# Optimization experiments

Hardware: AMD Instinct MI355X
Metric: run time of the kernel (lower is better)

## Reference

```python
import jax, jax.numpy as jnp
import numpy as np

B, N, K = 16, 2048, 20
EPS = 1e-5
SLOPE = 0.2  # LeakyReLU negative slope


def _lrelu(x):
    return jnp.where(x >= 0, x, SLOPE * x)


def _bn(x, g, b, axes):
    # BatchNorm in training mode (batch statistics), channel-last layout
    m = x.mean(axes, keepdims=True)
    v = x.var(axes, keepdims=True)
    return (x - m) * jax.lax.rsqrt(v + EPS) * g + b


def _graph_features(pts, k):
    # pts: [B, N, C] -> edge features [B, N, k, 2C] = concat(x_j - x_i, x_i)
    xx = jnp.sum(pts * pts, axis=-1)                       # [B, N]
    inner = jnp.einsum('bnc,bmc->bnm', pts, pts)           # [B, N, N]
    neg_d = 2.0 * inner - xx[:, :, None] - xx[:, None, :]  # -||x_i - x_j||^2
    _, idx = jax.lax.top_k(neg_d, k)                       # [B, N, k]
    xj = jax.vmap(lambda p, i: p[i])(pts, idx)             # [B, N, k, C]
    xi = pts[:, :, None, :]                                # [B, N, 1, C]
    return jnp.concatenate([xj - xi, jnp.broadcast_to(xi, xj.shape)], axis=-1)


def _forward(x, conv_w, conv_g, conv_b, w1, b1, g1, bt1, w2, b2, g2, bt2,
             w3, b3, g3, bt3, w4, b4, w5, b5):
    feat = _graph_features(x, K)                           # [B, N, K, 6]
    # 1x1 Conv2d (bias=False) + BN2d + LeakyReLU, then max over neighbors
    h = jnp.einsum('bnkc,oc->bnko', feat, conv_w)          # [B, N, K, 64]
    h = _lrelu(_bn(h, conv_g, conv_b, (0, 1, 2)))
    h = h.max(axis=2)                                      # [B, N, 64]
    # DBR blocks: Linear + BN1d + LeakyReLU over points
    h = _lrelu(_bn(h @ w1 + b1, g1, bt1, (0, 1)))          # [B, N, 64]
    h = _lrelu(_bn(h @ w2 + b2, g2, bt2, (0, 1)))          # [B, N, 128]
    h = _lrelu(_bn(h @ w3 + b3, g3, bt3, (0, 1)))          # [B, N, 128]
    h = h.max(axis=1)                                      # MaxChannel -> [B, 128]
    h = _lrelu(h @ w4 + b4)                                # DbR -> [B, 512]
    return h @ w5 + b5                                     # [B, 2*Z_DIM=256]


def setup_inputs() -> dict:
    key = jax.random.key(0)
    ks = jax.random.split(key, 8)
    rn = lambda k, s, sc: (jax.random.normal(k, s, jnp.float32) * sc)
    return {
        'x': jax.random.normal(ks[0], (B, N, 3), jnp.float32),
        'conv_w': rn(ks[1], (64, 6), 0.3),
        'conv_g': jnp.ones(64, jnp.float32), 'conv_b': jnp.zeros(64, jnp.float32),
        'w1': rn(ks[2], (64, 64), 0.1), 'b1': jnp.zeros(64, jnp.float32),
        'g1': jnp.ones(64, jnp.float32), 'bt1': jnp.zeros(64, jnp.float32),
        'w2': rn(ks[3], (64, 128), 0.1), 'b2': jnp.zeros(128, jnp.float32),
        'g2': jnp.ones(128, jnp.float32), 'bt2': jnp.zeros(128, jnp.float32),
        'w3': rn(ks[4], (128, 128), 0.1), 'b3': jnp.zeros(128, jnp.float32),
        'g3': jnp.ones(128, jnp.float32), 'bt3': jnp.zeros(128, jnp.float32),
        'w4': rn(ks[5], (128, 512), 0.05), 'b4': jnp.zeros(512, jnp.float32),
        'w5': rn(ks[6], (512, 256), 0.05), 'b5': jnp.zeros(256, jnp.float32),
    }


def reference(x, conv_w, conv_g, conv_b, w1, b1, g1, bt1, w2, b2, g2, bt2,
              w3, b3, g3, bt3, w4, b4, w5, b5):
    return _forward(x, conv_w, conv_g, conv_b, w1, b1, g1, bt1, w2, b2, g2, bt2,
                    w3, b3, g3, bt3, w4, b4, w5, b5)
```

## Files before the change

kernel.cpp:

```cpp
#include <hip/hip_runtime.h>
#include <math.h>

#define NB   16
#define NPTS 2048
#define KNBR 20
#define NCH  16
#define CHSZ (NPTS/NCH)
#define NROWS (NB*NPTS)
#define CONV_M ((double)(NB)*(double)(NPTS)*(double)(KNBR))
#define ROW_M  ((double)NROWS)
#define BN_EPS 1e-5
#define LSLOPE 0.2f

__device__ __forceinline__ float lrelu(float v) { return v >= 0.f ? v : LSLOPE * v; }

__device__ __forceinline__ float4 stage4(float px, float py, float pz)
{
    return make_float4(px + px, py + py, pz + pz,
                       -fmaf(px, px, fmaf(py, py, pz * pz)));
}

__device__ __forceinline__ float dist_eval(float4 q, float4 c)
{
    float t = fmaf(c.x, q.x, fmaf(c.y, q.y, fmaf(c.z, q.z, q.w)));
    return t + c.w;
}

__device__ __forceinline__ void pair_insert_sorted(float (&bestv)[KNBR], float t0, float t1)
{
#pragma unroll
    for (int j = 0; j < KNBR; ++j) {
        float bj = bestv[j];
        float nb  = fmaxf(bj, t0);
        float nt0 = __builtin_amdgcn_fmed3f(bj, t0, t1);
        float nt1 = fminf(bj, t1);
        bestv[j] = nb;
        t0 = nt0; t1 = nt1;
    }
}

__global__ __launch_bounds__(256) void knn_part(const float* __restrict__ x,
                                                float* __restrict__ P)
{
    __shared__ float4 cpt[2*CHSZ];
    __shared__ float4 qpt[256];
    const int b  = blockIdx.x >> 6;
    const int qg = (blockIdx.x >> 3) & 7;
    const int c0 = blockIdx.x & 7;
    const float* xb = x + (size_t)b * NPTS * 3;
    {
        const int half = threadIdx.x >> 7;
        const int jloc = threadIdx.x & (CHSZ - 1);
        const int j = (c0 + half*8) * CHSZ + jloc;
        cpt[threadIdx.x] = stage4(xb[j*3+0], xb[j*3+1], xb[j*3+2]);
        const int n = qg * 256 + threadIdx.x;
        float px = xb[n*3+0], py = xb[n*3+1], pz = xb[n*3+2];
        qpt[threadIdx.x] = make_float4(px, py, pz,
                                       -fmaf(px, px, fmaf(py, py, pz * pz)));
    }
    __syncthreads();
    const float4 q = qpt[threadIdx.x];
    float bA[KNBR], bB[KNBR];
#pragma unroll
    for (int j = 0; j < KNBR; ++j) { bA[j] = -__builtin_inff(); bB[j] = -__builtin_inff(); }
    for (int m = 0; m < CHSZ; m += 2) {
        float dA0 = dist_eval(q, cpt[m]);
        float dA1 = dist_eval(q, cpt[m+1]);
        float dB0 = dist_eval(q, cpt[CHSZ + m]);
        float dB1 = dist_eval(q, cpt[CHSZ + m+1]);
        float tA0 = fmaxf(dA0, dA1), tA1 = fminf(dA0, dA1);
        float tB0 = fmaxf(dB0, dB1), tB1 = fminf(dB0, dB1);
#pragma unroll
        for (int j = 0; j < KNBR; ++j) {
            float aj = bA[j], bj = bB[j];
            float nbA = fmaxf(aj, tA0);
            float nbB = fmaxf(bj, tB0);
            float nA0 = __builtin_amdgcn_fmed3f(aj, tA0, tA1);
            float nB0 = __builtin_amdgcn_fmed3f(bj, tB0, tB1);
            float nA1 = fminf(aj, tA1);
            float nB1 = fminf(bj, tB1);
            bA[j] = nbA; bB[j] = nbB;
            tA0 = nA0; tA1 = nA1; tB0 = nB0; tB1 = nB1;
        }
    }
    const size_t bq = (size_t)b * NPTS + qg * 256 + threadIdx.x;
#pragma unroll
    for (int i = 0; i < KNBR; ++i) {
        P[(size_t)(c0 * KNBR + i) * NROWS + bq]       = bA[i];
        P[(size_t)((c0+8) * KNBR + i) * NROWS + bq]   = bB[i];
    }
}

__global__ __launch_bounds__(256) void knn_merge(const float* __restrict__ P,
                                                 float* __restrict__ thresh)
{
    const size_t bq = (size_t)blockIdx.x * 256 + threadIdx.x;
    float bestv[KNBR];
#pragma unroll
    for (int j = 0; j < KNBR; ++j) bestv[j] = -__builtin_inff();
    for (int c = 0; c < NCH; ++c) {
        for (int i = 0; i < KNBR; i += 2) {
            float d0 = P[(size_t)(c * KNBR + i)     * NROWS + bq];
            float d1 = P[(size_t)(c * KNBR + i + 1) * NROWS + bq];
            if (!__any(d0 > bestv[KNBR-1])) break;
            pair_insert_sorted(bestv, d0, d1);
        }
    }
    thresh[bq] = bestv[KNBR-1];
}

__global__ __launch_bounds__(256) void idxfeat_kernel(const float* __restrict__ x,
        const float* __restrict__ thresh, const float* __restrict__ conv_w,
        float* __restrict__ maxh, float* __restrict__ minh, double* __restrict__ S)
{
    __shared__ float4 pts[NPTS];
    __shared__ unsigned short idxl[32][KNBR];
    __shared__ float  featw[4][KNBR][6];
    __shared__ double sred[4][27];
    const int b  = blockIdx.x >> 6;
    const int qg = blockIdx.x & 63;
    const int wv = threadIdx.x >> 6, lane = threadIdx.x & 63;
    const float* xb = x + (size_t)b * NPTS * 3;
    for (int i = threadIdx.x; i < NPTS; i += 256)
        pts[i] = stage4(xb[i*3+0], xb[i*3+1], xb[i*3+2]);
    __syncthreads();
    const unsigned long long below = (1ull << lane) - 1ull;
    for (int qi = 0; qi < 8; ++qi) {
        const int p = wv * 8 + qi;
        const int n = qg * 32 + p;
        const float4 qc = pts[n];
        const float4 q = make_float4(0.5f*qc.x, 0.5f*qc.y, 0.5f*qc.z, qc.w);
        const float th = thresh[(size_t)b * NPTS + n];
        int cnt = 0;
        for (int it = 0; it < NPTS/64; ++it) {
            float d = dist_eval(q, pts[it*64 + lane]);
            const bool hit = (d >= th);
            unsigned long long mask = __ballot(hit);
            int pos = cnt + __popcll(mask & below);
            if (hit && pos < KNBR)
                idxl[p][pos] = (unsigned short)(it*64 + lane);
            cnt += __popcll(mask);
        }
    }
    __syncthreads();
    float cw[6];
#pragma unroll
    for (int c = 0; c < 6; ++c) cw[c] = conv_w[lane*6 + c];
    int pa_ = 0, pb_ = 0;
    if (lane >= 6 && lane < 27) {
        int t = lane - 6, a = 0;
        while (t >= 6 - a) { t -= 6 - a; ++a; }
        pa_ = a; pb_ = a + t;
    }
    double acc = 0.0;
    for (int i = 0; i < 8; ++i) {
        const int p = wv * 8 + i;
        const int nn = qg * 32 + p;
        const size_t bp = (size_t)b * NPTS + nn;
        const float4 Ci = pts[nn];
        const float xi0 = 0.5f*Ci.x, xi1 = 0.5f*Ci.y, xi2 = 0.5f*Ci.z;
        float f0=0,f1=0,f2=0,f3=0,f4=0,f5=0;
        if (lane < KNBR) {
            const float4 Cj = pts[idxl[p][lane]];
            f0 = 0.5f*(Cj.x - Ci.x);
            f1 = 0.5f*(Cj.y - Ci.y);
            f2 = 0.5f*(Cj.z - Ci.z);
            f3 = xi0; f4 = xi1; f5 = xi2;
        }
        __syncthreads();
        if (lane < KNBR) {
            featw[wv][lane][0]=f0; featw[wv][lane][1]=f1; featw[wv][lane][2]=f2;
            featw[wv][lane][3]=f3; featw[wv][lane][4]=f4; featw[wv][lane][5]=f5;
        }
        __syncthreads();
        float vmax = -__builtin_inff(), vmin = __builtin_inff();
#pragma unroll
        for (int k = 0; k < KNBR; ++k) {
            float h = featw[wv][k][0] * cw[0];
            h = fmaf(featw[wv][k][1], cw[1], h);
            h = fmaf(featw[wv][k][2], cw[2], h);
            h = fmaf(featw[wv][k][3], cw[3], h);
            h = fmaf(featw[wv][k][4], cw[4], h);
            h = fmaf(featw[wv][k][5], cw[5], h);
            vmax = fmaxf(vmax, h); vmin = fminf(vmin, h);
        }
        maxh[bp*64 + lane] = vmax;
        minh[bp*64 + lane] = vmin;
        if (lane < 6) {
            double s = 0;
#pragma unroll
            for (int k = 0; k < KNBR; ++k) s += (double)featw[wv][k][lane];
            acc += s;
        } else if (lane < 27) {
            double s = 0;
#pragma unroll
            for (int k = 0; k < KNBR; ++k)
                s += (double)featw[wv][k][pa_] * (double)featw[wv][k][pb_];
            acc += s;
        }
    }
    if (lane < 27) sred[wv][lane] = acc;
    __syncthreads();
    if (threadIdx.x < 27) {
        double tot = sred[0][threadIdx.x] + sred[1][threadIdx.x]
                   + sred[2][threadIdx.x] + sred[3][threadIdx.x];
        atomicAdd(&S[threadIdx.x], tot);
    }
}

__global__ void stats0_kernel(const double* __restrict__ S, const float* __restrict__ conv_w,
        const float* __restrict__ g, const float* __restrict__ bb,
        float* __restrict__ scale, float* __restrict__ shift)
{
    const int o = threadIdx.x;
    double w[6];
#pragma unroll
    for (int c = 0; c < 6; ++c) w[c] = (double)conv_w[o*6 + c];
    double mean = 0.0;
#pragma unroll
    for (int c = 0; c < 6; ++c) mean += w[c] * S[c];
    mean /= CONV_M;
    double ey2 = 0.0;
    int t = 6;
#pragma unroll
    for (int a = 0; a < 6; ++a)
#pragma unroll
        for (int b2 = a; b2 < 6; ++b2) {
            double coef = (a == b2) ? 1.0 : 2.0;
            ey2 += coef * w[a] * w[b2] * S[t];
            ++t;
        }
    ey2 /= CONV_M;
    double var = ey2 - mean * mean;
    double sc = (double)g[o] / sqrt(var + BN_EPS);
    scale[o] = (float)sc;
    shift[o] = (float)((double)bb[o] - mean * sc);
}

__global__ void statsL_kernel(const double* __restrict__ sum, const double* __restrict__ sq,
        const float* __restrict__ g, const float* __restrict__ bt,
        float* __restrict__ scale, float* __restrict__ shift, int C)
{
    const int o = threadIdx.x;
    if (o >= C) return;
    double m = sum[o] / ROW_M;
    double v = sq[o] / ROW_M - m * m;
    double sc = (double)g[o] / sqrt(v + BN_EPS);
    scale[o] = (float)sc;
    shift[o] = (float)((double)bt[o] - m * sc);
}

template<int K, int N, bool SEL, bool POOLOUT>
__global__ __launch_bounds__(256) void mlp_gemm(const float* __restrict__ A,
        const float* __restrict__ A2, const float* __restrict__ sc_,
        const float* __restrict__ sh_, const float* __restrict__ W,
        const float* __restrict__ bias, float* __restrict__ Y,
        double* __restrict__ sum, double* __restrict__ sq,
        float* __restrict__ pmax_g, float* __restrict__ pmin_g)
{
    constexpr int CPT = N / 16;
    __shared__ float As[64 * 64];
    __shared__ float Ws[64 * N];
    const int tid = threadIdx.x;
    const int row0 = blockIdx.x * 64;
    const int ct = tid & 15, rt = tid >> 4;
    float acc[4][CPT];
#pragma unroll
    for (int rr = 0; rr < 4; ++rr)
#pragma unroll
        for (int cc = 0; cc < CPT; ++cc) acc[rr][cc] = bias[ct*CPT + cc];

    for (int kk = 0; kk < K/64; ++kk) {
        if (kk) __syncthreads();
#pragma unroll
        for (int i = 0; i < 4; ++i) {
            const int f   = i * 256 + tid;
            const int k4  = f & 15;
            const int row = f >> 4;
            const int kg  = kk*64 + k4*4;
            float4 m = *(const float4*)(A + (size_t)(row0+row)*K + kg);
            const float4 s4 = *(const float4*)(sc_ + kg);
            const float4 h4 = *(const float4*)(sh_ + kg);
            if (SEL) {
                float4 m2 = *(const float4*)(A2 + (size_t)(row0+row)*K + kg);
                m.x = s4.x >= 0.f ? m.x : m2.x;
                m.y = s4.y >= 0.f ? m.y : m2.y;
                m.z = s4.z >= 0.f ? m.z : m2.z;
                m.w = s4.w >= 0.f ? m.w : m2.w;
            }
            const int rsw = row ^ ((k4 & 7) << 2);
            As[(k4*4+0)*64 + rsw] = lrelu(fmaf(s4.x, m.x, h4.x));
            As[(k4*4+1)*64 + rsw] = lrelu(fmaf(s4.y, m.y, h4.y));
            As[(k4*4+2)*64 + rsw] = lrelu(fmaf(s4.z, m.z, h4.z));
            As[(k4*4+3)*64 + rsw] = lrelu(fmaf(s4.w, m.w, h4.w));
        }
#pragma unroll
        for (int i = 0; i < N/16; ++i) {
            const int f    = i * 256 + tid;
            const int col4 = f & (N/4 - 1);
            const int krow = f / (N/4);
            *(float4*)(&Ws[krow*N + col4*4]) =
                *(const float4*)(W + (size_t)(kk*64 + krow)*N + col4*4);
        }
        __syncthreads();
#pragma unroll 4
        for (int k = 0; k < 64; ++k) {
            const int sw = ((k >> 2) & 7) << 2;
            const float4 a0 = *(const float4*)(&As[k*64 + ((rt*4) ^ sw)]);
            float a_[4] = {a0.x, a0.y, a0.z, a0.w};
            float w_[CPT];
#pragma unroll
            for (int v = 0; v < CPT/4; ++v) {
                const float4 wv4 = *(const float4*)(&Ws[k*N + ct*CPT + v*4]);
                w_[v*4+0] = wv4.x; w_[v*4+1] = wv4.y; w_[v*4+2] = wv4.z; w_[v*4+3] = wv4.w;
            }
#pragma unroll
            for (int rr = 0; rr < 4; ++rr)
#pragma unroll
                for (int cc = 0; cc < CPT; ++cc)
                    acc[rr][cc] = fmaf(a_[rr], w_[cc], acc[rr][cc]);
        }
    }
    if (!POOLOUT) {
#pragma unroll
        for (int rr = 0; rr < 4; ++rr) {
            float* yo = Y + (size_t)(row0 + rt*4 + rr)*N + ct*CPT;
#pragma unroll
            for (int v = 0; v < CPT/4; ++v)
                *(float4*)(yo + v*4) = make_float4(acc[rr][v*4+0], acc[rr][v*4+1],
                                                   acc[rr][v*4+2], acc[rr][v*4+3]);
        }
    }
    __syncthreads();
    float* cr  = As;
    float* pmx = As + 512;
    float* pmn = Ws;
    if (tid < 2*N) cr[tid] = 0.f;
    if (POOLOUT) {
#pragma unroll
        for (int cc = 0; cc < CPT; ++cc) {
            float vmax = fmaxf(fmaxf(acc[0][cc], acc[1][cc]), fmaxf(acc[2][cc], acc[3][cc]));
            float vmin = fminf(fminf(acc[0][cc], acc[1][cc]), fminf(acc[2][cc], acc[3][cc]));
            pmx[rt*N + ct*CPT + cc] = vmax;
            pmn[rt*N + ct*CPT + cc] = vmin;
        }
    }
    __syncthreads();
#pragma unroll
    for (int cc = 0; cc < CPT; ++cc) {
        float s = acc[0][cc] + acc[1][cc] + acc[2][cc] + acc[3][cc];
        float q = fmaf(acc[0][cc], acc[0][cc], 0.f);
        q = fmaf(acc[1][cc], acc[1][cc], q);
        q = fmaf(acc[2][cc], acc[2][cc], q);
        q = fmaf(acc[3][cc], acc[3][cc], q);
        atomicAdd(&cr[ct*CPT + cc], s);
        atomicAdd(&cr[N + ct*CPT + cc], q);
    }
    float rm = 0.f, rn = 0.f;
    if (POOLOUT && tid < N) {
        rm = pmx[tid]; rn = pmn[tid];
#pragma unroll
        for (int r = 1; r < 16; ++r) {
            rm = fmaxf(rm, pmx[r*N + tid]);
            rn = fminf(rn, pmn[r*N + tid]);
        }
    }
    __syncthreads();
    if (tid < N) {
        atomicAdd(&sum[tid], (double)cr[tid]);
        atomicAdd(&sq[tid],  (double)cr[N + tid]);
        if (POOLOUT) {
            pmax_g[(size_t)blockIdx.x * N + tid] = rm;
            pmin_g[(size_t)blockIdx.x * N + tid] = rn;
        }
    }
}

__global__ __launch_bounds__(256) void headpool_kernel(const float* __restrict__ pmax_g,
        const float* __restrict__ pmin_g, const float* __restrict__ s3,
        const float* __restrict__ t3, const float* __restrict__ w4,
        const float* __restrict__ b4, const float* __restrict__ w5,
        const float* __restrict__ b5, float* __restrict__ out)
{
    __shared__ float xr[128];
    __shared__ float hh[512];
    const int b = blockIdx.x, t = threadIdx.x;
    if (t < 128) {
        const float* pm = pmax_g + (size_t)b * 32 * 128 + t;
        const float* pn = pmin_g + (size_t)b * 32 * 128 + t;
        float m = pm[0], n_ = pn[0];
#pragma unroll
        for (int r = 1; r < 32; ++r) {
            m  = fmaxf(m,  pm[r*128]);
            n_ = fminf(n_, pn[r*128]);
        }
        const float sc = s3[t], sh = t3[t];
        xr[t] = lrelu(sc >= 0.f ? fmaf(sc, m, sh) : fmaf(sc, n_, sh));
    }
    __syncthreads();
    float h0 = b4[t], h1 = b4[t + 256];
    for (int c = 0; c < 128; ++c) {
        float xc = xr[c];
        h0 = fmaf(xc, w4[c*512 + t],       h0);
        h1 = fmaf(xc, w4[c*512 + t + 256], h1);
    }
    hh[t]       = lrelu(h0);
    hh[t + 256] = lrelu(h1);
    __syncthreads();
    float acc = b5[t];
    for (int c = 0; c < 512; ++c)
        acc = fmaf(hh[c], w5[c*256 + t], acc);
    out[b*256 + t] = acc;
}

extern "C" void kernel_launch(void* const* d_in, const int* in_sizes, int n_in,
                              void* d_out, int out_size, void* d_ws, size_t ws_size,
                              hipStream_t stream)
{
    const float* x      = (const float*)d_in[0];
    const float* conv_w = (const float*)d_in[1];
    const float* conv_g = (const float*)d_in[2];
    const float* conv_b = (const float*)d_in[3];
    const float* w1  = (const float*)d_in[4];
    const float* b1  = (const float*)d_in[5];
    const float* g1  = (const float*)d_in[6];
    const float* bt1 = (const float*)d_in[7];
    const float* w2  = (const float*)d_in[8];
    const float* b2  = (const float*)d_in[9];
    const float* g2  = (const float*)d_in[10];
    const float* bt2 = (const float*)d_in[11];
    const float* w3  = (const float*)d_in[12];
    const float* b3  = (const float*)d_in[13];
    const float* g3  = (const float*)d_in[14];
    const float* bt3 = (const float*)d_in[15];
    const float* w4  = (const float*)d_in[16];
    const float* b4  = (const float*)d_in[17];
    const float* w5  = (const float*)d_in[18];
    const float* b5  = (const float*)d_in[19];

    char* p = (char*)d_ws;
    auto take = [&](size_t bytes) -> char* {
        char* r = p; p += (bytes + 255) & ~(size_t)255; return r;
    };
    double* S    = (double*)take(27 * 8);
    double* sum1 = (double*)take(64 * 8);
    double* sq1  = (double*)take(64 * 8);
    double* sum2 = (double*)take(128 * 8);
    double* sq2  = (double*)take(128 * 8);
    double* sum3 = (double*)take(128 * 8);
    double* sq3  = (double*)take(128 * 8);
    size_t zero_bytes = (size_t)(p - (char*)d_ws);
    float* scale0 = (float*)take(64 * 4);
    float* shift0 = (float*)take(64 * 4);
    float* scale1 = (float*)take(64 * 4);
    float* shift1 = (float*)take(64 * 4);
    float* scale2 = (float*)take(128 * 4);
    float* shift2 = (float*)take(128 * 4);
    float* scale3 = (float*)take(128 * 4);
    float* shift3 = (float*)take(128 * 4);
    float* pmaxg  = (float*)take((size_t)512 * 128 * 4);
    float* pming  = (float*)take((size_t)512 * 128 * 4);
    float* thresh = (float*)take((size_t)NROWS * 4);
    float* mm     = (float*)take((size_t)NROWS * 128 * 4);
    float* maxh   = mm;
    float* minh   = mm + (size_t)NROWS * 64;
    float* y1     = (float*)take((size_t)NROWS * 64 * 4);
    float* y2     = (float*)take((size_t)NROWS * 128 * 4);
    float* P      = mm;

    hipMemsetAsync(d_ws, 0, zero_bytes, stream);
    knn_part  <<<dim3(NB * 8 * 8),   dim3(256), 0, stream>>>(x, P);
    knn_merge <<<dim3(NROWS / 256),  dim3(256), 0, stream>>>(P, thresh);
    idxfeat_kernel<<<dim3(NB * 64),  dim3(256), 0, stream>>>(x, thresh, conv_w, maxh, minh, S);
    stats0_kernel<<<dim3(1),         dim3(64),  0, stream>>>(S, conv_w, conv_g, conv_b, scale0, shift0);

    mlp_gemm<64,64,true,false>   <<<dim3(512), dim3(256), 0, stream>>>(maxh, minh, scale0, shift0, w1, b1, y1, sum1, sq1, nullptr, nullptr);
    statsL_kernel                <<<dim3(1),   dim3(64),  0, stream>>>(sum1, sq1, g1, bt1, scale1, shift1, 64);
    mlp_gemm<64,128,false,false> <<<dim3(512), dim3(256), 0, stream>>>(y1, y1, scale1, shift1, w2, b2, y2, sum2, sq2, nullptr, nullptr);
    statsL_kernel                <<<dim3(1),   dim3(128), 0, stream>>>(sum2, sq2, g2, bt2, scale2, shift2, 128);
    mlp_gemm<128,128,false,true> <<<dim3(512), dim3(256), 0, stream>>>(y2, y2, scale2, shift2, w3, b3, nullptr, sum3, sq3, pmaxg, pming);
    statsL_kernel                <<<dim3(1),   dim3(128), 0, stream>>>(sum3, sq3, g3, bt3, scale3, shift3, 128);

    headpool_kernel<<<dim3(NB),      dim3(256), 0, stream>>>(pmaxg, pming, scale3, shift3, w4, b4, w5, b5, (float*)d_out);
}
```

Before: 409.1 us.

## Replace partial-sort kNN with per-wave radix bisection and fold BN stats into consumers

Drops the two-pass kNN (per-chunk top-20 insertion sort plus merge kernel). Each wavefront now keeps its query's 2048 distances in registers as order-preserving unsigned keys and bisects on the key value with ballot/popcount to find the 20th-largest threshold, then gathers indices as before. The separate BN statistics kernels are also removed: each GEMM block and the head kernel recompute scale/shift from the accumulated sums, which cuts launches and a global round trip. In exchange, every block redoes the small double-precision stats math, and the bisection can take up to 32 passes of 32 ballots per query while holding 32 key registers per lane.

```diff
diff --git a/kernel.cpp b/kernel.cpp
--- a/kernel.cpp
+++ b/kernel.cpp
@@ -4,8 +4,6 @@
 #define NB   16
 #define NPTS 2048
 #define KNBR 20
-#define NCH  16
-#define CHSZ (NPTS/NCH)
 #define NROWS (NB*NPTS)
 #define CONV_M ((double)(NB)*(double)(NPTS)*(double)(KNBR))
 #define ROW_M  ((double)NROWS)
@@ -26,91 +24,8 @@
     return t + c.w;
 }
 
-__device__ __forceinline__ void pair_insert_sorted(float (&bestv)[KNBR], float t0, float t1)
-{
-#pragma unroll
-    for (int j = 0; j < KNBR; ++j) {
-        float bj = bestv[j];
-        float nb  = fmaxf(bj, t0);
-        float nt0 = __builtin_amdgcn_fmed3f(bj, t0, t1);
-        float nt1 = fminf(bj, t1);
-        bestv[j] = nb;
-        t0 = nt0; t1 = nt1;
-    }
-}
-
-__global__ __launch_bounds__(256) void knn_part(const float* __restrict__ x,
-                                                float* __restrict__ P)
-{
-    __shared__ float4 cpt[2*CHSZ];
-    __shared__ float4 qpt[256];
-    const int b  = blockIdx.x >> 6;
-    const int qg = (blockIdx.x >> 3) & 7;
-    const int c0 = blockIdx.x & 7;
-    const float* xb = x + (size_t)b * NPTS * 3;
-    {
-        const int half = threadIdx.x >> 7;
-        const int jloc = threadIdx.x & (CHSZ - 1);
-        const int j = (c0 + half*8) * CHSZ + jloc;
-        cpt[threadIdx.x] = stage4(xb[j*3+0], xb[j*3+1], xb[j*3+2]);
-        const int n = qg * 256 + threadIdx.x;
-        float px = xb[n*3+0], py = xb[n*3+1], pz = xb[n*3+2];
-        qpt[threadIdx.x] = make_float4(px, py, pz,
-                                       -fmaf(px, px, fmaf(py, py, pz * pz)));
-    }
-    __syncthreads();
-    const float4 q = qpt[threadIdx.x];
-    float bA[KNBR], bB[KNBR];
-#pragma unroll
-    for (int j = 0; j < KNBR; ++j) { bA[j] = -__builtin_inff(); bB[j] = -__builtin_inff(); }
-    for (int m = 0; m < CHSZ; m += 2) {
-        float dA0 = dist_eval(q, cpt[m]);
-        float dA1 = dist_eval(q, cpt[m+1]);
-        float dB0 = dist_eval(q, cpt[CHSZ + m]);
-        float dB1 = dist_eval(q, cpt[CHSZ + m+1]);
-        float tA0 = fmaxf(dA0, dA1), tA1 = fminf(dA0, dA1);
-        float tB0 = fmaxf(dB0, dB1), tB1 = fminf(dB0, dB1);
-#pragma unroll
-        for (int j = 0; j < KNBR; ++j) {
-            float aj = bA[j], bj = bB[j];
-            float nbA = fmaxf(aj, tA0);
-            float nbB = fmaxf(bj, tB0);
-            float nA0 = __builtin_amdgcn_fmed3f(aj, tA0, tA1);
-            float nB0 = __builtin_amdgcn_fmed3f(bj, tB0, tB1);
-            float nA1 = fminf(aj, tA1);
-            float nB1 = fminf(bj, tB1);
-            bA[j] = nbA; bB[j] = nbB;
-            tA0 = nA0; tA1 = nA1; tB0 = nB0; tB1 = nB1;
-        }
-    }
-    const size_t bq = (size_t)b * NPTS + qg * 256 + threadIdx.x;
-#pragma unroll
-    for (int i = 0; i < KNBR; ++i) {
-        P[(size_t)(c0 * KNBR + i) * NROWS + bq]       = bA[i];
-        P[(size_t)((c0+8) * KNBR + i) * NROWS + bq]   = bB[i];
-    }
-}
-
-__global__ __launch_bounds__(256) void knn_merge(const float* __restrict__ P,
-                                                 float* __restrict__ thresh)
-{
-    const size_t bq = (size_t)blockIdx.x * 256 + threadIdx.x;
-    float bestv[KNBR];
-#pragma unroll
-    for (int j = 0; j < KNBR; ++j) bestv[j] = -__builtin_inff();
-    for (int c = 0; c < NCH; ++c) {
-        for (int i = 0; i < KNBR; i += 2) {
-            float d0 = P[(size_t)(c * KNBR + i)     * NROWS + bq];
-            float d1 = P[(size_t)(c * KNBR + i + 1) * NROWS + bq];
-            if (!__any(d0 > bestv[KNBR-1])) break;
-            pair_insert_sorted(bestv, d0, d1);
-        }
-    }
-    thresh[bq] = bestv[KNBR-1];
-}
-
-__global__ __launch_bounds__(256) void idxfeat_kernel(const float* __restrict__ x,
-        const float* __restrict__ thresh, const float* __restrict__ conv_w,
+__global__ __launch_bounds__(256) void knn_feat_kernel(const float* __restrict__ x,
+        const float* __restrict__ conv_w,
         float* __restrict__ maxh, float* __restrict__ minh, double* __restrict__ S)
 {
     __shared__ float4 pts[NPTS];
@@ -124,22 +39,52 @@
     for (int i = threadIdx.x; i < NPTS; i += 256)
         pts[i] = stage4(xb[i*3+0], xb[i*3+1], xb[i*3+2]);
     __syncthreads();
+
     const unsigned long long below = (1ull << lane) - 1ull;
     for (int qi = 0; qi < 8; ++qi) {
         const int p = wv * 8 + qi;
         const int n = qg * 32 + p;
         const float4 qc = pts[n];
         const float4 q = make_float4(0.5f*qc.x, 0.5f*qc.y, 0.5f*qc.z, qc.w);
-        const float th = thresh[(size_t)b * NPTS + n];
-        int cnt = 0;
-        for (int it = 0; it < NPTS/64; ++it) {
+        unsigned u[32];
+#pragma unroll
+        for (int it = 0; it < 32; ++it) {
             float d = dist_eval(q, pts[it*64 + lane]);
-            const bool hit = (d >= th);
+            unsigned bits = __float_as_uint(d);
+            u[it] = bits ^ (unsigned)(((int)bits >> 31) | (int)0x80000000);
+        }
+        unsigned lo = 0u, hi = 0xFFFFFFFFu;
+        for (int step = 0; step < 32; ++step) {
+            const unsigned mid = lo + ((hi - lo) >> 1);
+            int cnt = 0;
+#pragma unroll
+            for (int it = 0; it < 32; ++it)
+                cnt += __popcll(__ballot(u[it] >= mid));
+            if (cnt == KNBR) {
+                unsigned mn = 0xFFFFFFFFu;
+#pragma unroll
+                for (int it = 0; it < 32; ++it)
+                    mn = (u[it] >= mid && u[it] < mn) ? u[it] : mn;
+#pragma unroll
+                for (int o = 32; o >= 1; o >>= 1) {
+                    unsigned other = (unsigned)__shfl_xor((int)mn, o);
+                    mn = other < mn ? other : mn;
+                }
+                lo = mn;
+                break;
+            }
+            if (cnt > KNBR) lo = mid; else hi = mid;
+        }
+        const unsigned ustar = lo;
+        int cnt2 = 0;
+#pragma unroll
+        for (int it = 0; it < 32; ++it) {
+            const bool hit = (u[it] >= ustar);
             unsigned long long mask = __ballot(hit);
-            int pos = cnt + __popcll(mask & below);
+            int pos = cnt2 + __popcll(mask & below);
             if (hit && pos < KNBR)
                 idxl[p][pos] = (unsigned short)(it*64 + lane);
-            cnt += __popcll(mask);
+            cnt2 += __popcll(mask);
         }
     }
     __syncthreads();
@@ -208,60 +153,54 @@
     }
 }
 
-__global__ void stats0_kernel(const double* __restrict__ S, const float* __restrict__ conv_w,
-        const float* __restrict__ g, const float* __restrict__ bb,
-        float* __restrict__ scale, float* __restrict__ shift)
-{
-    const int o = threadIdx.x;
-    double w[6];
-#pragma unroll
-    for (int c = 0; c < 6; ++c) w[c] = (double)conv_w[o*6 + c];
-    double mean = 0.0;
-#pragma unroll
-    for (int c = 0; c < 6; ++c) mean += w[c] * S[c];
-    mean /= CONV_M;
-    double ey2 = 0.0;
-    int t = 6;
-#pragma unroll
-    for (int a = 0; a < 6; ++a)
-#pragma unroll
-        for (int b2 = a; b2 < 6; ++b2) {
-            double coef = (a == b2) ? 1.0 : 2.0;
-            ey2 += coef * w[a] * w[b2] * S[t];
-            ++t;
-        }
-    ey2 /= CONV_M;
-    double var = ey2 - mean * mean;
-    double sc = (double)g[o] / sqrt(var + BN_EPS);
-    scale[o] = (float)sc;
-    shift[o] = (float)((double)bb[o] - mean * sc);
-}
-
-__global__ void statsL_kernel(const double* __restrict__ sum, const double* __restrict__ sq,
-        const float* __restrict__ g, const float* __restrict__ bt,
-        float* __restrict__ scale, float* __restrict__ shift, int C)
-{
-    const int o = threadIdx.x;
-    if (o >= C) return;
-    double m = sum[o] / ROW_M;
-    double v = sq[o] / ROW_M - m * m;
-    double sc = (double)g[o] / sqrt(v + BN_EPS);
-    scale[o] = (float)sc;
-    shift[o] = (float)((double)bt[o] - m * sc);
-}
-
-template<int K, int N, bool SEL, bool POOLOUT>
+template<int K, int N, bool SEL, bool POOLOUT, bool STATS0>
 __global__ __launch_bounds__(256) void mlp_gemm(const float* __restrict__ A,
-        const float* __restrict__ A2, const float* __restrict__ sc_,
-        const float* __restrict__ sh_, const float* __restrict__ W,
-        const float* __restrict__ bias, float* __restrict__ Y,
-        double* __restrict__ sum, double* __restrict__ sq,
+        const float* __restrict__ A2,
+        const double* __restrict__ st_a, const double* __restrict__ st_b,
+        const float* __restrict__ st_g, const float* __restrict__ st_bt,
+        const float* __restrict__ cwm,
+        const float* __restrict__ W, const float* __restrict__ bias,
+        float* __restrict__ Y, double* __restrict__ sum, double* __restrict__ sq,
         float* __restrict__ pmax_g, float* __restrict__ pmin_g)
 {
     constexpr int CPT = N / 16;
     __shared__ float As[64 * 64];
     __shared__ float Ws[64 * N];
+    __shared__ __align__(16) float s_scale[K], s_shift[K];
     const int tid = threadIdx.x;
+    if (tid < K) {
+        const int o = tid;
+        if (STATS0) {
+            double w[6];
+#pragma unroll
+            for (int c = 0; c < 6; ++c) w[c] = (double)cwm[o*6 + c];
+            double mean = 0.0;
+#pragma unroll
+            for (int c = 0; c < 6; ++c) mean += w[c] * st_a[c];
+            mean /= CONV_M;
+            double ey2 = 0.0;
+            int t = 6;
+#pragma unroll
+            for (int a = 0; a < 6; ++a)
+#pragma unroll
+                for (int b2 = a; b2 < 6; ++b2) {
+                    double coef = (a == b2) ? 1.0 : 2.0;
+                    ey2 += coef * w[a] * w[b2] * st_a[t];
+                    ++t;
+                }
+            ey2 /= CONV_M;
+            double var = ey2 - mean * mean;
+            double sc = (double)st_g[o] / sqrt(var + BN_EPS);
+            s_scale[o] = (float)sc;
+            s_shift[o] = (float)((double)st_bt[o] - mean * sc);
+        } else {
+            double m = st_a[o] / ROW_M;
+            double v = st_b[o] / ROW_M - m * m;
+            double sc = (double)st_g[o] / sqrt(v + BN_EPS);
+            s_scale[o] = (float)sc;
+            s_shift[o] = (float)((double)st_bt[o] - m * sc);
+        }
+    }
     const int row0 = blockIdx.x * 64;
     const int ct = tid & 15, rt = tid >> 4;
     float acc[4][CPT];
@@ -269,6 +208,7 @@
     for (int rr = 0; rr < 4; ++rr)
 #pragma unroll
         for (int cc = 0; cc < CPT; ++cc) acc[rr][cc] = bias[ct*CPT + cc];
+    __syncthreads();
 
     for (int kk = 0; kk < K/64; ++kk) {
         if (kk) __syncthreads();
@@ -279,8 +219,8 @@
             const int row = f >> 4;
             const int kg  = kk*64 + k4*4;
             float4 m = *(const float4*)(A + (size_t)(row0+row)*K + kg);
-            const float4 s4 = *(const float4*)(sc_ + kg);
-            const float4 h4 = *(const float4*)(sh_ + kg);
+            const float4 s4 = *(const float4*)(&s_scale[kg]);
+            const float4 h4 = *(const float4*)(&s_shift[kg]);
             if (SEL) {
                 float4 m2 = *(const float4*)(A2 + (size_t)(row0+row)*K + kg);
                 m.x = s4.x >= 0.f ? m.x : m2.x;
@@ -377,15 +317,22 @@
 }
 
 __global__ __launch_bounds__(256) void headpool_kernel(const float* __restrict__ pmax_g,
-        const float* __restrict__ pmin_g, const float* __restrict__ s3,
-        const float* __restrict__ t3, const float* __restrict__ w4,
-        const float* __restrict__ b4, const float* __restrict__ w5,
-        const float* __restrict__ b5, float* __restrict__ out)
+        const float* __restrict__ pmin_g,
+        const double* __restrict__ sum3, const double* __restrict__ sq3,
+        const float* __restrict__ g3, const float* __restrict__ bt3,
+        const float* __restrict__ w4, const float* __restrict__ b4,
+        const float* __restrict__ w5, const float* __restrict__ b5,
+        float* __restrict__ out)
 {
     __shared__ float xr[128];
     __shared__ float hh[512];
     const int b = blockIdx.x, t = threadIdx.x;
     if (t < 128) {
+        double m_ = sum3[t] / ROW_M;
+        double v_ = sq3[t] / ROW_M - m_ * m_;
+        double scd = (double)g3[t] / sqrt(v_ + BN_EPS);
+        const float sc = (float)scd;
+        const float sh = (float)((double)bt3[t] - m_ * scd);
         const float* pm = pmax_g + (size_t)b * 32 * 128 + t;
         const float* pn = pmin_g + (size_t)b * 32 * 128 + t;
         float m = pm[0], n_ = pn[0];
@@ -394,7 +341,6 @@
             m  = fmaxf(m,  pm[r*128]);
             n_ = fminf(n_, pn[r*128]);
         }
-        const float sc = s3[t], sh = t3[t];
         xr[t] = lrelu(sc >= 0.f ? fmaf(sc, m, sh) : fmaf(sc, n_, sh));
     }
     __syncthreads();
@@ -450,36 +396,24 @@
     double* sum3 = (double*)take(128 * 8);
     double* sq3  = (double*)take(128 * 8);
     size_t zero_bytes = (size_t)(p - (char*)d_ws);
-    float* scale0 = (float*)take(64 * 4);
-    float* shift0 = (float*)take(64 * 4);
-    float* scale1 = (float*)take(64 * 4);
-    float* shift1 = (float*)take(64 * 4);
-    float* scale2 = (float*)take(128 * 4);
-    float* shift2 = (float*)take(128 * 4);
-    float* scale3 = (float*)take(128 * 4);
-    float* shift3 = (float*)take(128 * 4);
     float* pmaxg  = (float*)take((size_t)512 * 128 * 4);
     float* pming  = (float*)take((size_t)512 * 128 * 4);
-    float* thresh = (float*)take((size_t)NROWS * 4);
     float* mm     = (float*)take((size_t)NROWS * 128 * 4);
     float* maxh   = mm;
     float* minh   = mm + (size_t)NROWS * 64;
     float* y1     = (float*)take((size_t)NROWS * 64 * 4);
     float* y2     = (float*)take((size_t)NROWS * 128 * 4);
-    float* P      = mm;
 
     hipMemsetAsync(d_ws, 0, zero_bytes, stream);
-    knn_part  <<<dim3(NB * 8 * 8),   dim3(256), 0, stream>>>(x, P);
-    knn_merge <<<dim3(NROWS / 256),  dim3(256), 0, stream>>>(P, thresh);
-    idxfeat_kernel<<<dim3(NB * 64),  dim3(256), 0, stream>>>(x, thresh, conv_w, maxh, minh, S);
-    stats0_kernel<<<dim3(1),         dim3(64),  0, stream>>>(S, conv_w, conv_g, conv_b, scale0, shift0);
-
-    mlp_gemm<64,64,true,false>   <<<dim3(512), dim3(256), 0, stream>>>(maxh, minh, scale0, shift0, w1, b1, y1, sum1, sq1, nullptr, nullptr);
-    statsL_kernel                <<<dim3(1),   dim3(64),  0, stream>>>(sum1, sq1, g1, bt1, scale1, shift1, 64);
-    mlp_gemm<64,128,false,false> <<<dim3(512), dim3(256), 0, stream>>>(y1, y1, scale1, shift1, w2, b2, y2, sum2, sq2, nullptr, nullptr);
-    statsL_kernel                <<<dim3(1),   dim3(128), 0, stream>>>(sum2, sq2, g2, bt2, scale2, shift2, 128);
-    mlp_gemm<128,128,false,true> <<<dim3(512), dim3(256), 0, stream>>>(y2, y2, scale2, shift2, w3, b3, nullptr, sum3, sq3, pmaxg, pming);
-    statsL_kernel                <<<dim3(1),   dim3(128), 0, stream>>>(sum3, sq3, g3, bt3, scale3, shift3, 128);
-
-    headpool_kernel<<<dim3(NB),      dim3(256), 0, stream>>>(pmaxg, pming, scale3, shift3, w4, b4, w5, b5, (float*)d_out);
-}
+    knn_feat_kernel<<<dim3(NB * 64), dim3(256), 0, stream>>>(x, conv_w, maxh, minh, S);
+
+    mlp_gemm<64,64,true,false,true>    <<<dim3(512), dim3(256), 0, stream>>>(
+        maxh, minh, S, nullptr, conv_g, conv_b, conv_w, w1, b1, y1, sum1, sq1, nullptr, nullptr);
+    mlp_gemm<64,128,false,false,false> <<<dim3(512), dim3(256), 0, stream>>>(
+        y1, y1, sum1, sq1, g1, bt1, nullptr, w2, b2, y2, sum2, sq2, nullptr, nullptr);
+    mlp_gemm<128,128,false,true,false> <<<dim3(512), dim3(256), 0, stream>>>(
+        y2, y2, sum2, sq2, g2, bt2, nullptr, w3, b3, nullptr, sum3, sq3, pmaxg, pming);
+
+    headpool_kernel<<<dim3(NB), dim3(256), 0, stream>>>(
+        pmaxg, pming, sum3, sq3, g3, bt3, w4, b4, w5, b5, (float*)d_out);
+}
```

After: 391.5 us. 1.05x faster.
